# Kernel tuning notes

Measured on AMD Instinct MI355X. Metric: run time of the kernel, lower is better.

The kernel has to match this reference:

```python
import jax, jax.numpy as jnp
import numpy as np

T, H, E, K, I = 2048, 2048, 64, 8, 768
CAP = 512


def setup_inputs() -> dict:
    key = jax.random.key(0)
    ks = jax.random.split(key, 5)
    s = 0.02
    return {
        "hidden_states": jax.random.normal(ks[0], (T, H), jnp.float32),
        "w_router": jax.random.normal(ks[1], (E, H), jnp.float32) * s,
        "w_gate": jax.random.normal(ks[2], (E, H, I), jnp.float32) * s,
        "w_up": jax.random.normal(ks[3], (E, H, I), jnp.float32) * s,
        "w_down": jax.random.normal(ks[4], (E, I, H), jnp.float32) * s,
    }


def _moe(x, w_router, w_gate, w_up, w_down):
    Tn = x.shape[0]
    # --- router: softmax -> top-k -> renormalize (norm_topk_prob=True) ---
    logits = x @ w_router.T                                   # [T, E]
    probs = jax.nn.softmax(logits.astype(jnp.float32), axis=-1)
    topk_w, topk_idx = jax.lax.top_k(probs, K)                # [T, K]
    topk_w = topk_w / jnp.sum(topk_w, axis=-1, keepdims=True)
    # --- dispatch: sort (token, expert) pairs by expert, scatter into capacity buffers ---
    e = topk_idx.reshape(-1)                                  # [T*K] expert id per pair
    t = jnp.repeat(jnp.arange(Tn), K)                         # [T*K] token id per pair
    w = topk_w.reshape(-1)                                    # [T*K] combine weight per pair
    order = jnp.argsort(e, stable=True)
    e_s, t_s, w_s = e[order], t[order], w[order]
    counts = jax.ops.segment_sum(jnp.ones_like(e_s), e_s, num_segments=E)  # [E]
    starts = jnp.cumsum(counts) - counts                      # start offset of each expert group
    pos = jnp.arange(Tn * K) - starts[e_s]                    # slot within expert
    valid = pos < CAP
    posc = jnp.where(valid, pos, 0)
    vm = valid.astype(x.dtype)[:, None]
    buf = jnp.zeros((E, CAP, H), x.dtype).at[e_s, posc].add(x[t_s] * vm)   # [E, C, H]
    # --- grouped expert SwiGLU FFN: down(silu(gate(x)) * up(x)) ---
    g = jnp.einsum('ech,ehi->eci', buf, w_gate)               # [E, C, I]
    u = jnp.einsum('ech,ehi->eci', buf, w_up)                 # [E, C, I]
    y = jnp.einsum('eci,eih->ech', jax.nn.silu(g) * u, w_down)  # [E, C, H]
    # --- combine: gather expert outputs back to tokens, weighted sum ---
    gw = (w_s.astype(x.dtype) * valid.astype(x.dtype))[:, None]
    out = jnp.zeros((Tn, H), x.dtype).at[t_s].add(gw * y[e_s, posc])
    return out


def reference(hidden_states, w_router, w_gate, w_up, w_down):
    return _moe(hidden_states, w_router, w_gate, w_up, w_down)
```

## Files before the change

### kernel.cpp

```cpp
#include <hip/hip_runtime.h>
#include <hip/hip_bf16.h>
#include <math.h>

#define T_TOK 2048
#define H_DIM 2048
#define NEXP  64
#define TOPK  8
#define I_DIM 768
#define CAPE  512
#define MTMAX 4
#define LDW   40
#define YROWS 24576

typedef short bf16x8 __attribute__((ext_vector_type(8)));
typedef float f32x4  __attribute__((ext_vector_type(4)));

__device__ __forceinline__ unsigned short f2bf(float f) {
  unsigned u = __float_as_uint(f);
  u += 0x7fffu + ((u >> 16) & 1u);
  return (unsigned short)(u >> 16);
}
__device__ __forceinline__ float bf2f(unsigned short b) {
  return __uint_as_float(((unsigned)b) << 16);
}
__device__ __forceinline__ unsigned pack2(float lo, float hi) {
  __hip_bfloat162 h = __float22bfloat162_rn(make_float2(lo, hi));
  unsigned r; __builtin_memcpy(&r, &h, 4); return r;
}
__device__ __forceinline__ void lds_barrier() {
  asm volatile("s_waitcnt lgkmcnt(0)" ::: "memory");
  __builtin_amdgcn_s_barrier();
  __builtin_amdgcn_sched_barrier(0);
}

__global__ __launch_bounds__(256) void k_router(const float* __restrict__ x,
                                                const float* __restrict__ wr,
                                                int* __restrict__ topk_idx,
                                                float* __restrict__ topk_w) {
  const int lane = threadIdx.x & 63;
  const int t = blockIdx.x * 4 + (threadIdx.x >> 6);
  const float4* xr   = (const float4*)(x + (size_t)t * H_DIM);
  const float4* wrow = (const float4*)(wr + (size_t)lane * H_DIM);
  double acc = 0.0;
  for (int i = 0; i < H_DIM / 4; ++i) {
    float4 a = xr[i], b = wrow[i];
    acc += (double)a.x * b.x; acc += (double)a.y * b.y;
    acc += (double)a.z * b.z; acc += (double)a.w * b.w;
  }
  float cur = (float)acc;
  float val[TOPK]; int idx[TOPK];
#pragma unroll
  for (int r = 0; r < TOPK; ++r) {
    float bv = cur; int bi = lane;
#pragma unroll
    for (int off = 32; off > 0; off >>= 1) {
      float ov = __shfl_xor(bv, off);
      int   oi = __shfl_xor(bi, off);
      if (ov > bv || (ov == bv && oi < bi)) { bv = ov; bi = oi; }
    }
    val[r] = bv; idx[r] = bi;
    if (lane == bi) cur = -INFINITY;
  }
  float m = val[0], s = 0.f, w[TOPK];
#pragma unroll
  for (int r = 0; r < TOPK; ++r) { w[r] = expf(val[r] - m); s += w[r]; }
  if (lane < TOPK) {
    topk_idx[t * TOPK + lane] = idx[lane];
    topk_w [t * TOPK + lane] = w[lane] / s;
  }
}

__global__ __launch_bounds__(256) void k_rank(const int* __restrict__ topk_idx,
                                              int* __restrict__ pair_pos,
                                              int* __restrict__ slot_token,
                                              int* __restrict__ cnts,
                                              int* __restrict__ pstart) {
  __shared__ int s_run[64];
  __shared__ int s_whist[4][64];
  const int tid = threadIdx.x, lane = tid & 63, wv = tid >> 6;
  if (tid < 64) s_run[tid] = 0;
  for (int c = 0; c < 64; ++c) {
    const int p = c * 256 + tid;
    const int e = topk_idx[p];
    __syncthreads();
    s_whist[wv][lane] = 0;
    __syncthreads();
    unsigned long long m = ~0ull;
#pragma unroll
    for (int b = 0; b < 6; ++b) {
      unsigned long long bb = __ballot((e >> b) & 1);
      m &= ((e >> b) & 1) ? bb : ~bb;
    }
    const int rw = __popcll(m & ((1ull << lane) - 1ull));
    if (rw == 0) s_whist[wv][e] = __popcll(m);
    __syncthreads();
    int r = rw;
    for (int w2 = 0; w2 < wv; ++w2) r += s_whist[w2][e];
    const int pos = s_run[e] + r;
    pair_pos[p] = pos;
    if (pos < CAPE) slot_token[e * CAPE + pos] = p >> 3;
    __syncthreads();
    if (tid < 64)
      s_run[tid] += s_whist[0][tid] + s_whist[1][tid] + s_whist[2][tid] + s_whist[3][tid];
  }
  __syncthreads();
  if (tid < 64) cnts[tid] = s_run[tid];
  if (tid == 0) {
    int run = 0;
    for (int ee = 0; ee < 64; ++ee) {
      pstart[ee] = run;
      int c = s_run[ee]; if (c > CAPE) c = CAPE;
      run += (c + 127) & ~127;
    }
    pstart[64] = run;
  }
}

__global__ __launch_bounds__(256, 3) void k_mm1(const float* __restrict__ x,
                                                const float* __restrict__ wg,
                                                const float* __restrict__ wu,
                                                const int* __restrict__ slot_token,
                                                const int* __restrict__ cnts,
                                                unsigned short* __restrict__ gbuf,
                                                unsigned short* __restrict__ ubuf) {
  const int NB = NEXP * MTMAX * 12;
  const int v = (blockIdx.x & 7) * (NB / 8) + (blockIdx.x >> 3);
  const int e = v / (MTMAX * 12);
  const int rem = v % (MTMAX * 12);
  const int mt = rem / 12, nti = rem % 12;

  int cnt = cnts[e]; cnt = cnt < CAPE ? cnt : CAPE;
  if (cnt <= 0 || mt * 128 >= cnt) return;
  const int m0 = mt << 7;
  const float* wsrc = (nti < 6) ? wg : wu;
  unsigned short* obuf = (nti < 6) ? gbuf : ubuf;
  const int ncol = (nti % 6) * 128;

  __shared__ __align__(16) short As[2][128 * LDW];
  __shared__ __align__(16) short Bs[2][128 * LDW];

  const int tid = threadIdx.x;
  const int lane = tid & 63, wave = tid >> 6;
  const int wm = wave >> 1, wn = wave & 1;
  const int lr = lane & 15, lg = lane >> 4;

  const int a_row = tid >> 1, a_half = tid & 1;
  const int b_kp = tid & 15;
  const int b_nq0 = tid >> 4, b_nq1 = b_nq0 + 16;
  const size_t wbase = (size_t)e * H_DIM * I_DIM + (size_t)ncol;

  const int tok = (m0 + a_row < cnt) ? slot_token[e * CAPE + m0 + a_row] : 0;
  const float* xr = x + (size_t)tok * H_DIM + a_half * 16;
  const float* bp = wsrc + wbase + (size_t)(2 * b_kp) * I_DIM;

  f32x4 acc[4][4];
#pragma unroll
  for (int mi = 0; mi < 4; ++mi)
#pragma unroll
    for (int ni = 0; ni < 4; ++ni) acc[mi][ni] = (f32x4){0.f, 0.f, 0.f, 0.f};

  struct Tile { float4 a[4]; float4 b0[2]; float4 b1[2]; };
  Tile T;

  auto LOAD = [&](int kt) {
    const int k0 = kt * 32;
#pragma unroll
    for (int j = 0; j < 4; ++j) T.a[j] = *(const float4*)(xr + k0 + j * 4);
    const float* r0 = bp + (size_t)k0 * I_DIM;
    T.b0[0] = *(const float4*)(r0 + 4 * b_nq0);
    T.b0[1] = *(const float4*)(r0 + I_DIM + 4 * b_nq0);
    T.b1[0] = *(const float4*)(r0 + 4 * b_nq1);
    T.b1[1] = *(const float4*)(r0 + I_DIM + 4 * b_nq1);
  };
  auto STORE = [&](int b) {
    uint4 w0 = { pack2(T.a[0].x, T.a[0].y), pack2(T.a[0].z, T.a[0].w),
                 pack2(T.a[1].x, T.a[1].y), pack2(T.a[1].z, T.a[1].w) };
    uint4 w1 = { pack2(T.a[2].x, T.a[2].y), pack2(T.a[2].z, T.a[2].w),
                 pack2(T.a[3].x, T.a[3].y), pack2(T.a[3].z, T.a[3].w) };
    *(uint4*)(&As[b][a_row * LDW + a_half * 16])     = w0;
    *(uint4*)(&As[b][a_row * LDW + a_half * 16 + 8]) = w1;
    *(unsigned*)(&Bs[b][(4 * b_nq0 + 0) * LDW + 2 * b_kp]) = pack2(T.b0[0].x, T.b0[1].x);
    *(unsigned*)(&Bs[b][(4 * b_nq0 + 1) * LDW + 2 * b_kp]) = pack2(T.b0[0].y, T.b0[1].y);
    *(unsigned*)(&Bs[b][(4 * b_nq0 + 2) * LDW + 2 * b_kp]) = pack2(T.b0[0].z, T.b0[1].z);
    *(unsigned*)(&Bs[b][(4 * b_nq0 + 3) * LDW + 2 * b_kp]) = pack2(T.b0[0].w, T.b0[1].w);
    *(unsigned*)(&Bs[b][(4 * b_nq1 + 0) * LDW + 2 * b_kp]) = pack2(T.b1[0].x, T.b1[1].x);
    *(unsigned*)(&Bs[b][(4 * b_nq1 + 1) * LDW + 2 * b_kp]) = pack2(T.b1[0].y, T.b1[1].y);
    *(unsigned*)(&Bs[b][(4 * b_nq1 + 2) * LDW + 2 * b_kp]) = pack2(T.b1[0].z, T.b1[1].z);
    *(unsigned*)(&Bs[b][(4 * b_nq1 + 3) * LDW + 2 * b_kp]) = pack2(T.b1[0].w, T.b1[1].w);
  };
  auto COMPUTE = [&](int b) {
    bf16x8 af[4], bf[4];
#pragma unroll
    for (int mi = 0; mi < 4; ++mi)
      af[mi] = *(const bf16x8*)(&As[b][(wm * 64 + mi * 16 + lr) * LDW + lg * 8]);
#pragma unroll
    for (int ni = 0; ni < 4; ++ni)
      bf[ni] = *(const bf16x8*)(&Bs[b][(wn * 64 + ni * 16 + lr) * LDW + lg * 8]);
    __builtin_amdgcn_s_setprio(1);
#pragma unroll
    for (int mi = 0; mi < 4; ++mi)
#pragma unroll
      for (int ni = 0; ni < 4; ++ni)
        acc[mi][ni] = __builtin_amdgcn_mfma_f32_16x16x32_bf16(af[mi], bf[ni], acc[mi][ni], 0, 0, 0);
    __builtin_amdgcn_s_setprio(0);
  };

  const int NK = H_DIM / 32;
  LOAD(0); STORE(0); LOAD(1);
  lds_barrier();

#pragma unroll 1
  for (int t = 0; t + 2 < NK; t += 2) {
    COMPUTE(0); STORE(1); LOAD(t + 2);
    lds_barrier();
    COMPUTE(1); STORE(0); LOAD(t + 3);
    lds_barrier();
  }
  COMPUTE(0); STORE(1);
  lds_barrier();
  COMPUTE(1);

#pragma unroll
  for (int mi = 0; mi < 4; ++mi)
#pragma unroll
    for (int ni = 0; ni < 4; ++ni)
#pragma unroll
      for (int r = 0; r < 4; ++r) {
        const int row = m0 + wm * 64 + mi * 16 + lg * 4 + r;
        const int col = ncol + wn * 64 + ni * 16 + lr;
        obuf[(size_t)(e * CAPE + row) * I_DIM + col] = f2bf(acc[mi][ni][r]);
      }
}

__global__ __launch_bounds__(256) void k_act(unsigned short* __restrict__ gbuf,
                                             const unsigned short* __restrict__ ubuf,
                                             const int* __restrict__ cnts) {
  const int e = blockIdx.x >> 6;
  const int r0 = (blockIdx.x & 63) * 8;
  int cnt = cnts[e]; cnt = cnt < CAPE ? cnt : CAPE;
  const int lim = (cnt + 127) & ~127;
  if (r0 >= lim) return;
#pragma unroll
  for (int s = 0; s < 3; ++s) {
    const int c = threadIdx.x + 256 * s;
    const int row = r0 + c / 96;
    const int col = (c % 96) * 8;
    const size_t idx = (size_t)(e * CAPE + row) * I_DIM + col;
    bf16x8 g8 = *(const bf16x8*)(gbuf + idx);
    bf16x8 u8 = *(const bf16x8*)(ubuf + idx);
    bf16x8 o;
#pragma unroll
    for (int j = 0; j < 8; ++j) {
      const float g = bf2f((unsigned short)g8[j]);
      const float u = bf2f((unsigned short)u8[j]);
      o[j] = (short)f2bf((g / (1.f + __expf(-g))) * u);
    }
    *(bf16x8*)(gbuf + idx) = o;
  }
}

__global__ __launch_bounds__(256, 3) void k_down(const unsigned short* __restrict__ act,
                                                 const float* __restrict__ wd,
                                                 const int* __restrict__ cnts,
                                                 const int* __restrict__ pstart,
                                                 unsigned short* __restrict__ y) {
  const int NB = NEXP * MTMAX * 16;
  const int v = (blockIdx.x & 7) * (NB / 8) + (blockIdx.x >> 3);
  const int e = v / (MTMAX * 16);
  const int rem = v % (MTMAX * 16);
  const int mt = rem / 16, nt = rem % 16;

  int cnt = cnts[e]; cnt = cnt < CAPE ? cnt : CAPE;
  if (cnt <= 0 || mt * 128 >= cnt) return;
  const int m0 = mt << 7;
  const int ybase = pstart[e];
  if (ybase + m0 + 128 > YROWS) return;

  __shared__ __align__(16) short As[2][128 * LDW];
  __shared__ __align__(16) short Bs[2][128 * LDW];

  const int tid = threadIdx.x;
  const int lane = tid & 63, wave = tid >> 6;
  const int wm = wave >> 1, wn = wave & 1;
  const int lr = lane & 15, lg = lane >> 4;

  const int a_row = tid >> 1, a_half = tid & 1;
  const int b_kp = tid & 15;
  const int b_nq0 = tid >> 4, b_nq1 = b_nq0 + 16;
  const size_t wbase = (size_t)e * I_DIM * H_DIM + (size_t)nt * 128;

  const unsigned short* ap = act + (size_t)(e * CAPE + m0 + a_row) * I_DIM + a_half * 16;
  const float* bp = wd + wbase + (size_t)(2 * b_kp) * H_DIM;

  f32x4 acc[4][4];
#pragma unroll
  for (int mi = 0; mi < 4; ++mi)
#pragma unroll
    for (int ni = 0; ni < 4; ++ni) acc[mi][ni] = (f32x4){0.f, 0.f, 0.f, 0.f};

  struct Tile { bf16x8 a[2]; float4 b0[2]; float4 b1[2]; };
  Tile T;

  auto LOAD = [&](int kt) {
    const int k0 = kt * 32;
    T.a[0] = *(const bf16x8*)(ap + k0);
    T.a[1] = *(const bf16x8*)(ap + k0 + 8);
    const float* r0 = bp + (size_t)k0 * H_DIM;
    T.b0[0] = *(const float4*)(r0 + 4 * b_nq0);
    T.b0[1] = *(const float4*)(r0 + H_DIM + 4 * b_nq0);
    T.b1[0] = *(const float4*)(r0 + 4 * b_nq1);
    T.b1[1] = *(const float4*)(r0 + H_DIM + 4 * b_nq1);
  };
  auto STORE = [&](int b) {
    *(bf16x8*)(&As[b][a_row * LDW + a_half * 16])     = T.a[0];
    *(bf16x8*)(&As[b][a_row * LDW + a_half * 16 + 8]) = T.a[1];
    *(unsigned*)(&Bs[b][(4 * b_nq0 + 0) * LDW + 2 * b_kp]) = pack2(T.b0[0].x, T.b0[1].x);
    *(unsigned*)(&Bs[b][(4 * b_nq0 + 1) * LDW + 2 * b_kp]) = pack2(T.b0[0].y, T.b0[1].y);
    *(unsigned*)(&Bs[b][(4 * b_nq0 + 2) * LDW + 2 * b_kp]) = pack2(T.b0[0].z, T.b0[1].z);
    *(unsigned*)(&Bs[b][(4 * b_nq0 + 3) * LDW + 2 * b_kp]) = pack2(T.b0[0].w, T.b0[1].w);
    *(unsigned*)(&Bs[b][(4 * b_nq1 + 0) * LDW + 2 * b_kp]) = pack2(T.b1[0].x, T.b1[1].x);
    *(unsigned*)(&Bs[b][(4 * b_nq1 + 1) * LDW + 2 * b_kp]) = pack2(T.b1[0].y, T.b1[1].y);
    *(unsigned*)(&Bs[b][(4 * b_nq1 + 2) * LDW + 2 * b_kp]) = pack2(T.b1[0].z, T.b1[1].z);
    *(unsigned*)(&Bs[b][(4 * b_nq1 + 3) * LDW + 2 * b_kp]) = pack2(T.b1[0].w, T.b1[1].w);
  };
  auto COMPUTE = [&](int b) {
    bf16x8 af[4], bf[4];
#pragma unroll
    for (int mi = 0; mi < 4; ++mi)
      af[mi] = *(const bf16x8*)(&As[b][(wm * 64 + mi * 16 + lr) * LDW + lg * 8]);
#pragma unroll
    for (int ni = 0; ni < 4; ++ni)
      bf[ni] = *(const bf16x8*)(&Bs[b][(wn * 64 + ni * 16 + lr) * LDW + lg * 8]);
    __builtin_amdgcn_s_setprio(1);
#pragma unroll
    for (int mi = 0; mi < 4; ++mi)
#pragma unroll
      for (int ni = 0; ni < 4; ++ni)
        acc[mi][ni] = __builtin_amdgcn_mfma_f32_16x16x32_bf16(af[mi], bf[ni], acc[mi][ni], 0, 0, 0);
    __builtin_amdgcn_s_setprio(0);
  };

  const int NK = I_DIM / 32;
  LOAD(0); STORE(0); LOAD(1);
  lds_barrier();

#pragma unroll 1
  for (int t = 0; t + 2 < NK; t += 2) {
    COMPUTE(0); STORE(1); LOAD(t + 2);
    lds_barrier();
    COMPUTE(1); STORE(0); LOAD(t + 3);
    lds_barrier();
  }
  COMPUTE(0); STORE(1);
  lds_barrier();
  COMPUTE(1);

#pragma unroll
  for (int mi = 0; mi < 4; ++mi)
#pragma unroll
    for (int ni = 0; ni < 4; ++ni)
#pragma unroll
      for (int r = 0; r < 4; ++r) {
        const int row = ybase + m0 + wm * 64 + mi * 16 + lg * 4 + r;
        const int col = nt * 128 + wn * 64 + ni * 16 + lr;
        y[(size_t)row * H_DIM + col] = f2bf(acc[mi][ni][r]);
      }
}

__global__ __launch_bounds__(256) void k_combine(const unsigned short* __restrict__ y,
                                                 const int* __restrict__ topk_idx,
                                                 const float* __restrict__ topk_w,
                                                 const int* __restrict__ pair_pos,
                                                 const int* __restrict__ pstart,
                                                 float* __restrict__ out) {
  const int t = blockIdx.x;
  __shared__ int s_r[TOPK]; __shared__ float s_w[TOPK];
  if (threadIdx.x < TOPK) {
    const int e = topk_idx[t * TOPK + threadIdx.x];
    const int pos = pair_pos[t * TOPK + threadIdx.x];
    const int row = pstart[e] + pos;
    s_r[threadIdx.x] = (pos < CAPE && row < YROWS) ? row : -1;
    s_w[threadIdx.x] = topk_w[t * TOPK + threadIdx.x];
  }
  __syncthreads();
  const int h0 = threadIdx.x * 8;
  float acc[8] = {0.f, 0.f, 0.f, 0.f, 0.f, 0.f, 0.f, 0.f};
#pragma unroll
  for (int k = 0; k < TOPK; ++k) {
    const int row = s_r[k];
    if (row < 0) continue;
    const float w = s_w[k];
    const bf16x8 vv = *(const bf16x8*)(&y[(size_t)row * H_DIM + h0]);
#pragma unroll
    for (int j = 0; j < 8; ++j) acc[j] += w * bf2f((unsigned short)vv[j]);
  }
  float4 o0 = {acc[0], acc[1], acc[2], acc[3]};
  float4 o1 = {acc[4], acc[5], acc[6], acc[7]};
  *(float4*)(out + (size_t)t * H_DIM + h0)     = o0;
  *(float4*)(out + (size_t)t * H_DIM + h0 + 4) = o1;
}

extern "C" void kernel_launch(void* const* d_in, const int* in_sizes, int n_in,
                              void* d_out, int out_size, void* d_ws, size_t ws_size,
                              hipStream_t stream) {
  const float* x   = (const float*)d_in[0];
  const float* wr  = (const float*)d_in[1];
  const float* wgt = (const float*)d_in[2];
  const float* wup = (const float*)d_in[3];
  const float* wdn = (const float*)d_in[4];
  float* out = (float*)d_out;

  char* ws = (char*)d_ws;
  int*            topk_idx   = (int*)(ws);
  float*          topk_w     = (float*)(ws + 65536);
  int*            pair_pos   = (int*)(ws + 131072);
  int*            cnts       = (int*)(ws + 196608);
  int*            pstart     = (int*)(ws + 196864);
  int*            slot_token = (int*)(ws + 197376);
  unsigned short* gbuf       = (unsigned short*)(ws + 524288);
  unsigned short* ubuf       = (unsigned short*)(ws + 524288 + 50331648);
  unsigned short* yb         = (unsigned short*)(ws + 524288 + 50331648);

  k_router <<<dim3(T_TOK / 4),         dim3(256), 0, stream>>>(x, wr, topk_idx, topk_w);
  k_rank   <<<dim3(1),                 dim3(256), 0, stream>>>(topk_idx, pair_pos, slot_token, cnts, pstart);
  k_mm1    <<<dim3(NEXP * MTMAX * 12), dim3(256), 0, stream>>>(x, wgt, wup, slot_token, cnts, gbuf, ubuf);
  k_act    <<<dim3(NEXP * 64),         dim3(256), 0, stream>>>(gbuf, ubuf, cnts);
  k_down   <<<dim3(NEXP * MTMAX * 16), dim3(256), 0, stream>>>(gbuf, wdn, cnts, pstart, yb);
  k_combine<<<dim3(T_TOK),             dim3(256), 0, stream>>>(yb, topk_idx, topk_w, pair_pos, pstart, out);
}
```

Measured before the change: 859.2 us.

## Double-buffer register prefetch and issue loads before MFMA in expert GEMMs

Both grouped GEMM kernels now hold two register tiles, so the global load for the tile two steps ahead is issued before the MFMA compute of the current tile. A sched_barrier stops the compiler from sinking those loads past the compute, which gives memory latency more time to hide. The block-index decode is also reordered so that consecutive blocks share an expert and N-tile while stepping through M-tiles, improving L2 reuse of weights. The extra register tile raises VGPR pressure, which could reduce occupancy under launch_bounds(256,3).

```diff
diff --git a/kernel.cpp b/kernel.cpp
--- a/kernel.cpp
+++ b/kernel.cpp
@@ -125,9 +125,9 @@
                                                 unsigned short* __restrict__ ubuf) {
   const int NB = NEXP * MTMAX * 12;
   const int v = (blockIdx.x & 7) * (NB / 8) + (blockIdx.x >> 3);
-  const int e = v / (MTMAX * 12);
-  const int rem = v % (MTMAX * 12);
-  const int mt = rem / 12, nti = rem % 12;
+  const int mt = v & 3;
+  const int nti = (v >> 2) % 12;
+  const int e = v / 48;
 
   int cnt = cnts[e]; cnt = cnt < CAPE ? cnt : CAPE;
   if (cnt <= 0 || mt * 128 >= cnt) return;
@@ -160,9 +160,9 @@
     for (int ni = 0; ni < 4; ++ni) acc[mi][ni] = (f32x4){0.f, 0.f, 0.f, 0.f};
 
   struct Tile { float4 a[4]; float4 b0[2]; float4 b1[2]; };
-  Tile T;
-
-  auto LOAD = [&](int kt) {
+  Tile tA, tB;
+
+  auto LOAD = [&](Tile& T, int kt) {
     const int k0 = kt * 32;
 #pragma unroll
     for (int j = 0; j < 4; ++j) T.a[j] = *(const float4*)(xr + k0 + j * 4);
@@ -171,8 +171,9 @@
     T.b0[1] = *(const float4*)(r0 + I_DIM + 4 * b_nq0);
     T.b1[0] = *(const float4*)(r0 + 4 * b_nq1);
     T.b1[1] = *(const float4*)(r0 + I_DIM + 4 * b_nq1);
-  };
-  auto STORE = [&](int b) {
+    __builtin_amdgcn_sched_barrier(0);
+  };
+  auto STORE = [&](const Tile& T, int b) {
     uint4 w0 = { pack2(T.a[0].x, T.a[0].y), pack2(T.a[0].z, T.a[0].w),
                  pack2(T.a[1].x, T.a[1].y), pack2(T.a[1].z, T.a[1].w) };
     uint4 w1 = { pack2(T.a[2].x, T.a[2].y), pack2(T.a[2].z, T.a[2].w),
@@ -206,17 +207,23 @@
   };
 
   const int NK = H_DIM / 32;
-  LOAD(0); STORE(0); LOAD(1);
+  LOAD(tA, 0); LOAD(tB, 1);
+  STORE(tA, 0);
   lds_barrier();
 
 #pragma unroll 1
-  for (int t = 0; t + 2 < NK; t += 2) {
-    COMPUTE(0); STORE(1); LOAD(t + 2);
+  for (int t = 0; t + 3 < NK; t += 2) {
+    LOAD(tA, t + 2);
+    COMPUTE(0);
+    STORE(tB, 1);
     lds_barrier();
-    COMPUTE(1); STORE(0); LOAD(t + 3);
+    LOAD(tB, t + 3);
+    COMPUTE(1);
+    STORE(tA, 0);
     lds_barrier();
   }
-  COMPUTE(0); STORE(1);
+  COMPUTE(0);
+  STORE(tB, 1);
   lds_barrier();
   COMPUTE(1);
 
@@ -266,9 +273,9 @@
                                                  unsigned short* __restrict__ y) {
   const int NB = NEXP * MTMAX * 16;
   const int v = (blockIdx.x & 7) * (NB / 8) + (blockIdx.x >> 3);
-  const int e = v / (MTMAX * 16);
-  const int rem = v % (MTMAX * 16);
-  const int mt = rem / 16, nt = rem % 16;
+  const int mt = v & 3;
+  const int nt = (v >> 2) & 15;
+  const int e = v >> 6;
 
   int cnt = cnts[e]; cnt = cnt < CAPE ? cnt : CAPE;
   if (cnt <= 0 || mt * 128 >= cnt) return;
@@ -299,9 +306,9 @@
     for (int ni = 0; ni < 4; ++ni) acc[mi][ni] = (f32x4){0.f, 0.f, 0.f, 0.f};
 
   struct Tile { bf16x8 a[2]; float4 b0[2]; float4 b1[2]; };
-  Tile T;
-
-  auto LOAD = [&](int kt) {
+  Tile tA, tB;
+
+  auto LOAD = [&](Tile& T, int kt) {
     const int k0 = kt * 32;
     T.a[0] = *(const bf16x8*)(ap + k0);
     T.a[1] = *(const bf16x8*)(ap + k0 + 8);
@@ -310,8 +317,9 @@
     T.b0[1] = *(const float4*)(r0 + H_DIM + 4 * b_nq0);
     T.b1[0] = *(const float4*)(r0 + 4 * b_nq1);
     T.b1[1] = *(const float4*)(r0 + H_DIM + 4 * b_nq1);
-  };
-  auto STORE = [&](int b) {
+    __builtin_amdgcn_sched_barrier(0);
+  };
+  auto STORE = [&](const Tile& T, int b) {
     *(bf16x8*)(&As[b][a_row * LDW + a_half * 16])     = T.a[0];
     *(bf16x8*)(&As[b][a_row * LDW + a_half * 16 + 8]) = T.a[1];
     *(unsigned*)(&Bs[b][(4 * b_nq0 + 0) * LDW + 2 * b_kp]) = pack2(T.b0[0].x, T.b0[1].x);
@@ -341,17 +349,23 @@
   };
 
   const int NK = I_DIM / 32;
-  LOAD(0); STORE(0); LOAD(1);
+  LOAD(tA, 0); LOAD(tB, 1);
+  STORE(tA, 0);
   lds_barrier();
 
 #pragma unroll 1
-  for (int t = 0; t + 2 < NK; t += 2) {
-    COMPUTE(0); STORE(1); LOAD(t + 2);
+  for (int t = 0; t + 3 < NK; t += 2) {
+    LOAD(tA, t + 2);
+    COMPUTE(0);
+    STORE(tB, 1);
     lds_barrier();
-    COMPUTE(1); STORE(0); LOAD(t + 3);
+    LOAD(tB, t + 3);
+    COMPUTE(1);
+    STORE(tA, 0);
     lds_barrier();
   }
-  COMPUTE(0); STORE(1);
+  COMPUTE(0);
+  STORE(tB, 1);
   lds_barrier();
   COMPUTE(1);
 
```

Result: slower. 1.102 ms (+28.2%).
